# Performance work log

Measured on AMD Instinct MI355X. Metric: run time of the kernel, lower is better.

The kernel has to match this reference:

```python
import jax, jax.numpy as jnp
import numpy as np

S, B, E = 2048, 2, 1024   # seq, batch, hidden (transpose_batch_sequence=True -> [S,B,E])
H, D = 16, 64             # num_heads, head_dim; H*D == E
EPS = 1e-6


def setup_inputs() -> dict:
    key = jax.random.key(0)
    k1, k2, k3 = jax.random.split(key, 3)
    x = jax.random.normal(k1, (S, B, E), dtype=jnp.float32)
    ln_scale = jnp.ones((E,), dtype=jnp.float32)
    # variance-scaling fan_in init ~ N(0, 1/fan_in); query block scaled by 1/sqrt(head_dim)
    w_qkv = jax.random.normal(k2, (E, 3 * H * D), dtype=jnp.float32) / np.sqrt(E)
    w_qkv = w_qkv.at[:, : H * D].divide(np.sqrt(D))  # scaled_query_init
    w_out = jax.random.normal(k3, (H * D, E), dtype=jnp.float32) / np.sqrt(H * D)
    return {"x": x, "ln_scale": ln_scale, "w_qkv": w_qkv, "w_out": w_out}


def reference(x, ln_scale, w_qkv, w_out):
    # LayerNormDenseGeneral: layernorm (scale only) fused with QKV projection
    mu = jnp.mean(x, axis=-1, keepdims=True)
    var = jnp.mean(jnp.square(x - mu), axis=-1, keepdims=True)
    ln = (x - mu) * jax.lax.rsqrt(var + EPS) * ln_scale          # [S,B,E]
    qkv = jnp.einsum('sbe,ef->sbf', ln, w_qkv)                    # [S,B,3HD]
    q, k, v = jnp.split(qkv, 3, axis=-1)
    q = q.reshape(S, B, H, D)
    k = k.reshape(S, B, H, D)
    v = v.reshape(S, B, H, D)
    # core_attention (transpose_batch_sequence=True): full score matrix
    attn = jnp.einsum('qbhd,kbhd->bhqk', q, k)                    # [B,H,S,S]
    attn = jax.nn.softmax(attn, axis=-1)
    ctx = jnp.einsum('bhqk,kbhd->qbhd', attn, v)                  # [S,B,H,D]
    ctx = ctx.reshape(S, B, H * D)
    out = jnp.einsum('sbf,fe->sbe', ctx, w_out)                   # output projection
    return out
```

## Files before the change

kernel.cpp:

```cpp
#include <hip/hip_runtime.h>
#include <math.h>


typedef unsigned short u16;
typedef unsigned int u32;
typedef __bf16 bf16x8 __attribute__((ext_vector_type(8)));
typedef float f32x4 __attribute__((ext_vector_type(4)));
typedef u16 u16x8 __attribute__((ext_vector_type(8)));
typedef u16 u16x4 __attribute__((ext_vector_type(4)));
typedef u16 u16x2 __attribute__((ext_vector_type(2)));
typedef u32 u32x2 __attribute__((ext_vector_type(2)));

#define S_LEN 2048
#define BATCH 2
#define EDIM  1024
#define NHEAD 16
#define DHEAD 64
#define MROWS 4096
#define NQKV  3072
#define KDIM  1024
#define LOG2E 1.4426950408889634f

__device__ __forceinline__ float bf2f(u16 u) {
  union { unsigned int u; float f; } v; v.u = ((unsigned int)u) << 16; return v.f;
}
__device__ __forceinline__ u16 f2bf(float f) {
  union { float f; unsigned int u; } v; v.f = f;
  return (u16)((v.u + 0x7FFFu + ((v.u >> 16) & 1u)) >> 16);
}
__device__ __forceinline__ u32 cvt_pk_bf16(float lo, float hi) {
  u32 r;
  asm("v_cvt_pk_bf16_f32 %0, %1, %2" : "=v"(r) : "v"(lo), "v"(hi));
  return r;
}
__device__ __forceinline__ void glds16(const void* g, void* l) {
  __builtin_amdgcn_global_load_lds((__attribute__((address_space(1))) void*)g,
                                   (__attribute__((address_space(3))) void*)l,
                                   16, 0, 0);
}

__global__ __launch_bounds__(256) void prep_kernel(const void* __restrict__ xv,
                                                   const void* __restrict__ scv,
                                                   const void* __restrict__ wqv,
                                                   const void* __restrict__ wov,
                                                   u16* __restrict__ lnb,
                                                   u16* __restrict__ wqkvT,
                                                   u16* __restrict__ woutT) {
  const int t = threadIdx.x;
  const u16 dv = ((const u16*)xv)[t & 63];
  const int de = (dv >> 7) & 0xFF;
  const unsigned long long dm = __ballot(de >= 100 && de <= 140);
  const int isbf = (__popcll(dm) >= 56) ? 1 : 0;
  const int bid = blockIdx.x;

  if (bid < MROWS) {
    const int row = bid;
    float v0, v1, v2, v3;
    if (isbf) {
      u16x4 xin = *(const u16x4*)((const u16*)xv + (size_t)row * EDIM + t * 4);
      v0 = bf2f(xin[0]); v1 = bf2f(xin[1]); v2 = bf2f(xin[2]); v3 = bf2f(xin[3]);
    } else {
      float4 xin = *(const float4*)((const float*)xv + (size_t)row * EDIM + t * 4);
      v0 = xin.x; v1 = xin.y; v2 = xin.z; v3 = xin.w;
    }
    float s  = v0 + v1 + v2 + v3;
    float ss = v0 * v0 + v1 * v1 + v2 * v2 + v3 * v3;
    #pragma unroll
    for (int off = 1; off < 64; off <<= 1) {
      s  += __shfl_xor(s, off);
      ss += __shfl_xor(ss, off);
    }
    __shared__ float ps[4], pq[4];
    const int w = t >> 6;
    if ((t & 63) == 0) { ps[w] = s; pq[w] = ss; }
    __syncthreads();
    s  = ps[0] + ps[1] + ps[2] + ps[3];
    ss = pq[0] + pq[1] + pq[2] + pq[3];
    const float mu   = s * (1.0f / EDIM);
    const float rstd = rsqrtf(ss * (1.0f / EDIM) - mu * mu + 1e-6f);
    float sc0, sc1, sc2, sc3;
    if (isbf) {
      const u16* sc = (const u16*)scv + t * 4;
      sc0 = bf2f(sc[0]); sc1 = bf2f(sc[1]); sc2 = bf2f(sc[2]); sc3 = bf2f(sc[3]);
    } else {
      const float* sc = (const float*)scv + t * 4;
      sc0 = sc[0]; sc1 = sc[1]; sc2 = sc[2]; sc3 = sc[3];
    }
    u16x4 o;
    o[0] = f2bf((v0 - mu) * rstd * sc0);
    o[1] = f2bf((v1 - mu) * rstd * sc1);
    o[2] = f2bf((v2 - mu) * rstd * sc2);
    o[3] = f2bf((v3 - mu) * rstd * sc3);
    *(u16x4*)(lnb + (size_t)row * EDIM + t * 4) = o;
  } else {
    __shared__ u16 tile[32][33];
    int gx, gy, R, C, scaleCols;
    const void* inv; u16* out;
    if (bid < MROWS + 3072) {
      const int idx = bid - MROWS;
      gx = idx % 96; gy = idx / 96;
      R = KDIM; C = NQKV; scaleCols = 1024; inv = wqv; out = wqkvT;
    } else {
      const int idx = bid - MROWS - 3072;
      gx = idx & 31; gy = idx >> 5;
      R = EDIM; C = EDIM; scaleCols = 0; inv = wov; out = woutT;
    }
    const int tx = t & 31, ty = t >> 5;
    const int c0 = gx * 32, r0 = gy * 32;
    const float scale = (c0 + tx < scaleCols) ? LOG2E : 1.0f;
    #pragma unroll
    for (int i = 0; i < 4; ++i) {
      const int r = r0 + ty + i * 8;
      float fv;
      if (isbf) fv = bf2f(((const u16*)inv)[(size_t)r * C + c0 + tx]);
      else      fv = ((const float*)inv)[(size_t)r * C + c0 + tx];
      tile[ty + i * 8][tx] = f2bf(fv * scale);
    }
    __syncthreads();
    #pragma unroll
    for (int i = 0; i < 4; ++i)
      out[(size_t)(c0 + ty + i * 8) * R + r0 + tx] = tile[tx][ty + i * 8];
  }
}

template <int OUT_F32, int V_EP>
__global__ __launch_bounds__(256) void gemm_bt(const u16* __restrict__ A,
                                               const u16* __restrict__ Bt,
                                               void* __restrict__ Cv,
                                               const int N,
                                               u16* __restrict__ vT) {
  __shared__ __align__(16) u16 pool[2][2][128][32];
  const int t = threadIdx.x;
  const int w = t >> 6, lane = t & 63;
  const int quad = lane >> 4, l16 = lane & 15;
  const int gdx = gridDim.x;
  const int nwg = gdx * gridDim.y;
  const int flat = blockIdx.y * gdx + blockIdx.x;
  const int nf = (flat & 7) * (nwg >> 3) + (flat >> 3);
  const int bn = (nf % gdx) * 128, bm = (nf / gdx) * 128;
  const int wm = (w >> 1) * 64, wn = (w & 1) * 64;
  const int arow = lane >> 2, aseg = (lane & 3) * 8;
  f32x4 acc[4][4] = {};
  const u16* Ab = A  + (size_t)(bm + arow) * KDIM + aseg;
  const u16* Bb = Bt + (size_t)(bn + arow) * KDIM + aseg;
  #pragma unroll
  for (int i = 0; i < 2; ++i) {
    const int rb = w * 32 + i * 16;
    glds16(Ab + (size_t)rb * KDIM, &pool[0][0][rb][0]);
    glds16(Bb + (size_t)rb * KDIM, &pool[1][0][rb][0]);
  }
  __syncthreads();
  int cur = 0;
  for (int kt = 0; kt < KDIM; kt += 32) {
    if (kt + 32 < KDIM) {
      #pragma unroll
      for (int i = 0; i < 2; ++i) {
        const int rb = w * 32 + i * 16;
        glds16(Ab + (size_t)rb * KDIM + kt + 32, &pool[0][cur ^ 1][rb][0]);
        glds16(Bb + (size_t)rb * KDIM + kt + 32, &pool[1][cur ^ 1][rb][0]);
      }
    }
    bf16x8 af[4], bfv[4];
    #pragma unroll
    for (int mt = 0; mt < 4; ++mt) af[mt]  = *(const bf16x8*)&pool[0][cur][wm + mt * 16 + l16][quad * 8];
    #pragma unroll
    for (int nt = 0; nt < 4; ++nt) bfv[nt] = *(const bf16x8*)&pool[1][cur][wn + nt * 16 + l16][quad * 8];
    #pragma unroll
    for (int mt = 0; mt < 4; ++mt)
      #pragma unroll
      for (int nt = 0; nt < 4; ++nt)
        acc[mt][nt] = __builtin_amdgcn_mfma_f32_16x16x32_bf16(af[mt], bfv[nt], acc[mt][nt], 0, 0, 0);
    __syncthreads();
    cur ^= 1;
  }

  if (V_EP && bn >= 2048) {
    u16* scr = &pool[0][0][0][0];
    #pragma unroll
    for (int mt = 0; mt < 4; ++mt)
      #pragma unroll
      for (int nt = 0; nt < 4; ++nt) {
        const int col = wn + nt * 16 + l16;
        const int hh = col >> 6, dd = col & 63;
        const int unit = (wm >> 2) + mt * 4 + quad;
        const int up = (((unit >> 2) ^ (dd & 7)) << 2) + (unit & 3);
        const int base = (hh * 64 + dd) * 128;
        u16x2 e0, e1;
        e0[0] = f2bf(acc[mt][nt][0]); e0[1] = f2bf(acc[mt][nt][2]);
        e1[0] = f2bf(acc[mt][nt][1]); e1[1] = f2bf(acc[mt][nt][3]);
        *(u16x2*)&scr[base + up * 2]      = e0;
        *(u16x2*)&scr[base + 64 + up * 2] = e1;
      }
    __syncthreads();
    const int s0 = bm >> 1;
    const int hbase = (bn - 2048) >> 6;
    #pragma unroll
    for (int i = 0; i < 8; ++i) {
      const int cid = i * 256 + t;
      const int u4 = cid & 7;
      const int b  = (cid >> 3) & 1;
      const int dd = (cid >> 4) & 63;
      const int hh = cid >> 10;
      const u16x8 val = *(const u16x8*)&scr[(hh * 64 + dd) * 128 + b * 64 + ((u4 ^ (dd & 7)) << 3)];
      *(u16x8*)&vT[(size_t)((b * 16 + hbase + hh) * 64 + dd) * S_LEN + s0 + u4 * 8] = val;
    }
    return;
  }

  #pragma unroll
  for (int mt = 0; mt < 4; ++mt)
    #pragma unroll
    for (int nt = 0; nt < 4; ++nt)
      #pragma unroll
      for (int r = 0; r < 4; ++r) {
        const int row = bm + wm + mt * 16 + quad * 4 + r;
        const int col = bn + wn + nt * 16 + l16;
        if (OUT_F32) ((float*)Cv)[(size_t)row * N + col] = acc[mt][nt][r];
        else         ((u16*)Cv)[(size_t)row * N + col] = f2bf(acc[mt][nt][r]);
      }
}

__global__ __launch_bounds__(256) void attn_kernel(const u16* __restrict__ qkv,
                                                   const u16* __restrict__ vT,
                                                   u16* __restrict__ ctx) {
  __shared__ __align__(16) u16 Ks[2][64][64];
  __shared__ __align__(16) u16 Vs[2][64][64];
  __shared__ __align__(16) u16 Ps[64][64];
  const int t = threadIdx.x;
  const int w = t >> 6, lane = t & 63;
  const int quad = lane >> 4, l16 = lane & 15;
  const int flat = blockIdx.y * gridDim.x + blockIdx.x;
  const int nf = (flat & 7) * 128 + (flat >> 3);
  const int q0 = (nf & 31) * 64;
  const int bh = nf >> 5, b = bh >> 4, h = bh & 15;
  const u16* qbase = qkv + h * DHEAD;
  const u16* kbase = qkv + EDIM + h * DHEAD;
  const u16* vbase = vT + (size_t)bh * DHEAD * S_LEN;

  bf16x8 qf[2];
  #pragma unroll
  for (int ks = 0; ks < 2; ++ks)
    qf[ks] = *(const bf16x8*)(qbase + (size_t)((q0 + w * 16 + l16) * 2 + b) * NQKV + ks * 32 + quad * 8);

  const int srow = lane >> 3;
  const int schk = (lane & 7) ^ srow;
  const int rdswz = (l16 & 7);
  const int pswz = (l16 & 7) * 2;

  bf16x8 onesf;
  #pragma unroll
  for (int j = 0; j < 8; ++j) onesf[j] = (__bf16)1.0f;

  f32x4 oacc[4] = {};
  f32x4 sacc = {};

  #pragma unroll
  for (int i = 0; i < 2; ++i) {
    const int rb = (w * 2 + i) * 8;
    const int row = rb + srow;
    glds16(kbase + (size_t)(row * 2 + b) * NQKV + schk * 8, &Ks[0][rb][0]);
    glds16(vbase + (size_t)row * S_LEN + schk * 8, &Vs[0][rb][0]);
  }
  __syncthreads();

  for (int kc = 0; kc < S_LEN / 64; ++kc) {
    const int nb = kc & 1;
    if (kc + 1 < S_LEN / 64) {
      #pragma unroll
      for (int i = 0; i < 2; ++i) {
        const int rb = (w * 2 + i) * 8;
        const int row = rb + srow;
        glds16(kbase + (size_t)(((kc + 1) * 64 + row) * 2 + b) * NQKV + schk * 8, &Ks[nb ^ 1][rb][0]);
        glds16(vbase + (size_t)row * S_LEN + (kc + 1) * 64 + schk * 8, &Vs[nb ^ 1][rb][0]);
      }
    }
    bf16x8 kf[4][2];
    #pragma unroll
    for (int nt = 0; nt < 4; ++nt)
      #pragma unroll
      for (int ks = 0; ks < 2; ++ks)
        kf[nt][ks] = *(const bf16x8*)&Ks[nb][nt * 16 + l16][((ks * 4 + quad) ^ rdswz) * 8];
    f32x4 sa[4] = {};
    #pragma unroll
    for (int ks = 0; ks < 2; ++ks)
      #pragma unroll
      for (int nt = 0; nt < 4; ++nt)
        sa[nt] = __builtin_amdgcn_mfma_f32_16x16x32_bf16(kf[nt][ks], qf[ks], sa[nt], 0, 0, 0);
    #pragma unroll
    for (int nt = 0; nt < 4; ++nt) {
      const float p0 = exp2f(sa[nt][0]);
      const float p1 = exp2f(sa[nt][1]);
      const float p2 = exp2f(sa[nt][2]);
      const float p3 = exp2f(sa[nt][3]);
      u32x2 pw;
      pw[0] = cvt_pk_bf16(p0, p1);
      pw[1] = cvt_pk_bf16(p2, p3);
      *(u32x2*)&Ps[w * 16 + l16][(((nt * 4 + quad) ^ pswz) & 15) * 4] = pw;
    }
    bf16x8 vf[4][2];
    #pragma unroll
    for (int nd = 0; nd < 4; ++nd)
      #pragma unroll
      for (int ks = 0; ks < 2; ++ks)
        vf[nd][ks] = *(const bf16x8*)&Vs[nb][nd * 16 + l16][((ks * 4 + quad) ^ rdswz) * 8];
    asm volatile("s_waitcnt lgkmcnt(0)" ::: "memory");
    __builtin_amdgcn_sched_barrier(0);
    bf16x8 pf0 = *(const bf16x8*)&Ps[w * 16 + l16][(((quad * 2) ^ pswz) & 15) * 4];
    bf16x8 pf1 = *(const bf16x8*)&Ps[w * 16 + l16][(((8 + quad * 2) ^ pswz) & 15) * 4];
    #pragma unroll
    for (int nd = 0; nd < 4; ++nd) {
      oacc[nd] = __builtin_amdgcn_mfma_f32_16x16x32_bf16(pf0, vf[nd][0], oacc[nd], 0, 0, 0);
      oacc[nd] = __builtin_amdgcn_mfma_f32_16x16x32_bf16(pf1, vf[nd][1], oacc[nd], 0, 0, 0);
    }
    sacc = __builtin_amdgcn_mfma_f32_16x16x32_bf16(pf0, onesf, sacc, 0, 0, 0);
    sacc = __builtin_amdgcn_mfma_f32_16x16x32_bf16(pf1, onesf, sacc, 0, 0, 0);
    __syncthreads();
  }
  #pragma unroll
  for (int r = 0; r < 4; ++r) {
    const float inv = 1.0f / sacc[r];
    const int srowq = q0 + w * 16 + quad * 4 + r;
    #pragma unroll
    for (int nd = 0; nd < 4; ++nd) {
      const int col = h * DHEAD + nd * 16 + l16;
      ctx[(size_t)(srowq * 2 + b) * EDIM + col] = f2bf(oacc[nd][r] * inv);
    }
  }
}

extern "C" void kernel_launch(void* const* d_in, const int* in_sizes, int n_in,
                              void* d_out, int out_size, void* d_ws, size_t ws_size,
                              hipStream_t stream) {
  const void* x = nullptr; const void* sc = nullptr;
  const void* wq = nullptr; const void* wo = nullptr;
  for (int i = 0; i < n_in; ++i) {
    switch (in_sizes[i]) {
      case 4194304: x  = d_in[i]; break;
      case 1024:    sc = d_in[i]; break;
      case 3145728: wq = d_in[i]; break;
      case 1048576: wo = d_in[i]; break;
      default: break;
    }
  }
  if (!x)  x  = d_in[0];
  if (!sc) sc = d_in[1];
  if (!wq) wq = d_in[2];
  if (!wo) wo = d_in[3];

  char* ws = (char*)d_ws;
  u16* lnb   = (u16*)(ws);
  u16* wqkvT = (u16*)(ws + 8388608);
  u16* woutT = (u16*)(ws + 14680064);
  u16* qkv   = (u16*)(ws + 16777216);
  u16* vT    = (u16*)(ws + 41943040);
  u16* ctx   = (u16*)(ws + 50331648);

  prep_kernel<<<MROWS + 3072 + 1024, 256, 0, stream>>>(x, sc, wq, wo, lnb, wqkvT, woutT);
  gemm_bt<0, 1><<<dim3(NQKV / 128, MROWS / 128), 256, 0, stream>>>(lnb, wqkvT, qkv, NQKV, vT);
  attn_kernel<<<dim3(S_LEN / 64, BATCH * NHEAD), 256, 0, stream>>>(qkv, vT, ctx);
  gemm_bt<1, 0><<<dim3(EDIM / 128, MROWS / 128), 256, 0, stream>>>(ctx, woutT, d_out, EDIM, nullptr);
}
```

Baseline: 194.7 us.

## Keep softmax probabilities in registers and permute V reads to match MFMA layout

```diff
diff --git a/kernel.cpp b/kernel.cpp
--- a/kernel.cpp
+++ b/kernel.cpp
@@ -5,11 +5,12 @@
 typedef unsigned short u16;
 typedef unsigned int u32;
 typedef __bf16 bf16x8 __attribute__((ext_vector_type(8)));
+typedef __bf16 bf16x4 __attribute__((ext_vector_type(4)));
 typedef float f32x4 __attribute__((ext_vector_type(4)));
 typedef u16 u16x8 __attribute__((ext_vector_type(8)));
 typedef u16 u16x4 __attribute__((ext_vector_type(4)));
 typedef u16 u16x2 __attribute__((ext_vector_type(2)));
-typedef u32 u32x2 __attribute__((ext_vector_type(2)));
+typedef u32 u32x4 __attribute__((ext_vector_type(4)));
 
 #define S_LEN 2048
 #define BATCH 2
@@ -225,7 +226,6 @@
                                                    u16* __restrict__ ctx) {
   __shared__ __align__(16) u16 Ks[2][64][64];
   __shared__ __align__(16) u16 Vs[2][64][64];
-  __shared__ __align__(16) u16 Ps[64][64];
   const int t = threadIdx.x;
   const int w = t >> 6, lane = t & 63;
   const int quad = lane >> 4, l16 = lane & 15;
@@ -245,7 +245,6 @@
   const int srow = lane >> 3;
   const int schk = (lane & 7) ^ srow;
   const int rdswz = (l16 & 7);
-  const int pswz = (l16 & 7) * 2;
 
   bf16x8 onesf;
   #pragma unroll
@@ -286,31 +285,35 @@
       #pragma unroll
       for (int nt = 0; nt < 4; ++nt)
         sa[nt] = __builtin_amdgcn_mfma_f32_16x16x32_bf16(kf[nt][ks], qf[ks], sa[nt], 0, 0, 0);
+    union { u32x4 u; bf16x8 b; } pk0, pk1;
     #pragma unroll
     for (int nt = 0; nt < 4; ++nt) {
       const float p0 = exp2f(sa[nt][0]);
       const float p1 = exp2f(sa[nt][1]);
       const float p2 = exp2f(sa[nt][2]);
       const float p3 = exp2f(sa[nt][3]);
-      u32x2 pw;
-      pw[0] = cvt_pk_bf16(p0, p1);
-      pw[1] = cvt_pk_bf16(p2, p3);
-      *(u32x2*)&Ps[w * 16 + l16][(((nt * 4 + quad) ^ pswz) & 15) * 4] = pw;
-    }
-    bf16x8 vf[4][2];
-    #pragma unroll
-    for (int nd = 0; nd < 4; ++nd)
-      #pragma unroll
-      for (int ks = 0; ks < 2; ++ks)
-        vf[nd][ks] = *(const bf16x8*)&Vs[nb][nd * 16 + l16][((ks * 4 + quad) ^ rdswz) * 8];
-    asm volatile("s_waitcnt lgkmcnt(0)" ::: "memory");
-    __builtin_amdgcn_sched_barrier(0);
-    bf16x8 pf0 = *(const bf16x8*)&Ps[w * 16 + l16][(((quad * 2) ^ pswz) & 15) * 4];
-    bf16x8 pf1 = *(const bf16x8*)&Ps[w * 16 + l16][(((8 + quad * 2) ^ pswz) & 15) * 4];
+      if (nt < 2) {
+        pk0.u[(nt & 1) * 2]     = cvt_pk_bf16(p0, p1);
+        pk0.u[(nt & 1) * 2 + 1] = cvt_pk_bf16(p2, p3);
+      } else {
+        pk1.u[(nt & 1) * 2]     = cvt_pk_bf16(p0, p1);
+        pk1.u[(nt & 1) * 2 + 1] = cvt_pk_bf16(p2, p3);
+      }
+    }
+    const bf16x8 pf0 = pk0.b;
+    const bf16x8 pf1 = pk1.b;
     #pragma unroll
     for (int nd = 0; nd < 4; ++nd) {
-      oacc[nd] = __builtin_amdgcn_mfma_f32_16x16x32_bf16(pf0, vf[nd][0], oacc[nd], 0, 0, 0);
-      oacc[nd] = __builtin_amdgcn_mfma_f32_16x16x32_bf16(pf1, vf[nd][1], oacc[nd], 0, 0, 0);
+      const u16* vrow = &Vs[nb][nd * 16 + l16][0];
+      #pragma unroll
+      for (int ks = 0; ks < 2; ++ks) {
+        const bf16x4 va = *(const bf16x4*)&vrow[(((ks * 4 + (quad >> 1)) ^ rdswz) << 3) + (quad & 1) * 4];
+        const bf16x4 vb = *(const bf16x4*)&vrow[(((ks * 4 + 2 + (quad >> 1)) ^ rdswz) << 3) + (quad & 1) * 4];
+        bf16x8 v8;
+        v8[0] = va[0]; v8[1] = va[1]; v8[2] = va[2]; v8[3] = va[3];
+        v8[4] = vb[0]; v8[5] = vb[1]; v8[6] = vb[2]; v8[7] = vb[3];
+        oacc[nd] = __builtin_amdgcn_mfma_f32_16x16x32_bf16(ks ? pf1 : pf0, v8, oacc[nd], 0, 0, 0);
+      }
     }
     sacc = __builtin_amdgcn_mfma_f32_16x16x32_bf16(pf0, onesf, sacc, 0, 0, 0);
     sacc = __builtin_amdgcn_mfma_f32_16x16x32_bf16(pf1, onesf, sacc, 0, 0, 0);
```

Measured after the change: 202.3 us. 1.04x slower.

## Software-pipeline attention loop: compute next tile's QK scores during current PV

Applied to the files above, without the earlier changes.

```diff
diff --git a/kernel.cpp b/kernel.cpp
--- a/kernel.cpp
+++ b/kernel.cpp
@@ -260,32 +260,33 @@
     const int row = rb + srow;
     glds16(kbase + (size_t)(row * 2 + b) * NQKV + schk * 8, &Ks[0][rb][0]);
     glds16(vbase + (size_t)row * S_LEN + schk * 8, &Vs[0][rb][0]);
+    glds16(kbase + (size_t)((64 + row) * 2 + b) * NQKV + schk * 8, &Ks[1][rb][0]);
+    glds16(vbase + (size_t)row * S_LEN + 64 + schk * 8, &Vs[1][rb][0]);
   }
   __syncthreads();
-
-  for (int kc = 0; kc < S_LEN / 64; ++kc) {
-    const int nb = kc & 1;
-    if (kc + 1 < S_LEN / 64) {
-      #pragma unroll
-      for (int i = 0; i < 2; ++i) {
-        const int rb = (w * 2 + i) * 8;
-        const int row = rb + srow;
-        glds16(kbase + (size_t)(((kc + 1) * 64 + row) * 2 + b) * NQKV + schk * 8, &Ks[nb ^ 1][rb][0]);
-        glds16(vbase + (size_t)row * S_LEN + (kc + 1) * 64 + schk * 8, &Vs[nb ^ 1][rb][0]);
-      }
-    }
+  f32x4 sa[4] = {};
+  {
     bf16x8 kf[4][2];
     #pragma unroll
     for (int nt = 0; nt < 4; ++nt)
       #pragma unroll
       for (int ks = 0; ks < 2; ++ks)
-        kf[nt][ks] = *(const bf16x8*)&Ks[nb][nt * 16 + l16][((ks * 4 + quad) ^ rdswz) * 8];
-    f32x4 sa[4] = {};
+        kf[nt][ks] = *(const bf16x8*)&Ks[0][nt * 16 + l16][((ks * 4 + quad) ^ rdswz) * 8];
     #pragma unroll
     for (int ks = 0; ks < 2; ++ks)
       #pragma unroll
       for (int nt = 0; nt < 4; ++nt)
         sa[nt] = __builtin_amdgcn_mfma_f32_16x16x32_bf16(kf[nt][ks], qf[ks], sa[nt], 0, 0, 0);
+  }
+
+  for (int tc = 0; tc < S_LEN / 64; ++tc) {
+    const int cur = tc & 1;
+    bf16x8 vf[4][2];
+    #pragma unroll
+    for (int nd = 0; nd < 4; ++nd)
+      #pragma unroll
+      for (int ks = 0; ks < 2; ++ks)
+        vf[nd][ks] = *(const bf16x8*)&Vs[cur][nd * 16 + l16][((ks * 4 + quad) ^ rdswz) * 8];
     #pragma unroll
     for (int nt = 0; nt < 4; ++nt) {
       const float p0 = exp2f(sa[nt][0]);
@@ -297,12 +298,30 @@
       pw[1] = cvt_pk_bf16(p2, p3);
       *(u32x2*)&Ps[w * 16 + l16][(((nt * 4 + quad) ^ pswz) & 15) * 4] = pw;
     }
-    bf16x8 vf[4][2];
-    #pragma unroll
-    for (int nd = 0; nd < 4; ++nd)
+    __syncthreads();
+    if (tc + 2 < S_LEN / 64) {
+      #pragma unroll
+      for (int i = 0; i < 2; ++i) {
+        const int rb = (w * 2 + i) * 8;
+        const int row = rb + srow;
+        glds16(kbase + (size_t)(((tc + 2) * 64 + row) * 2 + b) * NQKV + schk * 8, &Ks[cur][rb][0]);
+        glds16(vbase + (size_t)row * S_LEN + (tc + 2) * 64 + schk * 8, &Vs[cur][rb][0]);
+      }
+    }
+    f32x4 sn[4] = {};
+    if (tc + 1 < S_LEN / 64) {
+      bf16x8 kf[4][2];
+      #pragma unroll
+      for (int nt = 0; nt < 4; ++nt)
+        #pragma unroll
+        for (int ks = 0; ks < 2; ++ks)
+          kf[nt][ks] = *(const bf16x8*)&Ks[cur ^ 1][nt * 16 + l16][((ks * 4 + quad) ^ rdswz) * 8];
       #pragma unroll
       for (int ks = 0; ks < 2; ++ks)
-        vf[nd][ks] = *(const bf16x8*)&Vs[nb][nd * 16 + l16][((ks * 4 + quad) ^ rdswz) * 8];
+        #pragma unroll
+        for (int nt = 0; nt < 4; ++nt)
+          sn[nt] = __builtin_amdgcn_mfma_f32_16x16x32_bf16(kf[nt][ks], qf[ks], sn[nt], 0, 0, 0);
+    }
     asm volatile("s_waitcnt lgkmcnt(0)" ::: "memory");
     __builtin_amdgcn_sched_barrier(0);
     bf16x8 pf0 = *(const bf16x8*)&Ps[w * 16 + l16][(((quad * 2) ^ pswz) & 15) * 4];
@@ -314,7 +333,8 @@
     }
     sacc = __builtin_amdgcn_mfma_f32_16x16x32_bf16(pf0, onesf, sacc, 0, 0, 0);
     sacc = __builtin_amdgcn_mfma_f32_16x16x32_bf16(pf1, onesf, sacc, 0, 0, 0);
-    __syncthreads();
+    #pragma unroll
+    for (int nt = 0; nt < 4; ++nt) sa[nt] = sn[nt];
   }
   #pragma unroll
   for (int r = 0; r < 4; ++r) {
```

After: 206.0 us. +5.8%, slower.
